# Performance work log

Hardware: AMD Instinct MI355X
Metric: run time of the kernel (lower is better)

The kernel has to match this reference:

```python
import jax, jax.numpy as jnp
import numpy as np

N = 50000      # nodes
DEG = 16       # uniform degree -> E = N*DEG edges
E = N * DEG
D_IN = 256
D_OUT = 128


def setup_inputs() -> dict:
    key = jax.random.key(0)
    k_x, k_w, k_col = jax.random.split(key, 3)
    X = jax.random.normal(k_x, (N, D_IN), dtype=jnp.float32)
    weights = jax.random.normal(k_w, (D_IN, D_OUT), dtype=jnp.float32)
    # CSR adjacency: uniform degree for simplicity; row_pointers[i] = i*DEG
    row_pointers = (jnp.arange(N + 1, dtype=jnp.int32) * DEG)
    column_index = jax.random.randint(k_col, (E,), 0, N, dtype=jnp.int32)
    # Kernel tiling metadata (unused by the math; placeholders)
    n_blk = 3125
    blockPartition = jnp.ones((n_blk,), dtype=jnp.int32)
    edgeToColumn = jnp.zeros((E,), dtype=jnp.int32)
    edgeToRow = jnp.zeros((E,), dtype=jnp.int32)
    hybrid_type = jnp.zeros((n_blk,), dtype=jnp.int32)
    row_nzr = jnp.zeros((N,), dtype=jnp.int32)
    col_nzr = jnp.zeros((E,), dtype=jnp.int32)
    return {
        "X": X,
        "weights": weights,
        "row_pointers": row_pointers,
        "column_index": column_index,
        "blockPartition": blockPartition,
        "edgeToColumn": edgeToColumn,
        "edgeToRow": edgeToRow,
        "hybrid_type": hybrid_type,
        "row_nzr": row_nzr,
        "col_nzr": col_nzr,
    }


def reference(X, weights, row_pointers, column_index, blockPartition,
              edgeToColumn, edgeToRow, hybrid_type, row_nzr, col_nzr):
    # GCNConv (fixed=0): X' = X @ W, then block-sparse SpMM A @ X' where A is the
    # unweighted CSR adjacency (sum over in-neighbors).
    Xp = jnp.matmul(X, weights)  # [N, D_OUT]
    n = X.shape[0]
    e = column_index.shape[0]
    # Recover per-edge destination row from CSR row_pointers.
    edge_dst = jnp.searchsorted(row_pointers, jnp.arange(e, dtype=row_pointers.dtype),
                                side="right").astype(jnp.int32) - 1  # [E]
    gathered = Xp[column_index]  # [E, D_OUT] irregular gather
    out = jax.ops.segment_sum(gathered, edge_dst, num_segments=n)  # [N, D_OUT]
    return out
```

## Files before the change

kernel.cpp:

```cpp
#include <hip/hip_runtime.h>
#include <hip/hip_bf16.h>


constexpr int D_IN  = 256;
constexpr int D_OUT = 128;
constexpr int BM = 128;
constexpr int BK = 32;
constexpr int LDA = BK + 8;

using short8  = __attribute__((ext_vector_type(8))) short;
using float4v = __attribute__((ext_vector_type(4))) float;

__device__ inline ushort f2bf(float f) {
    unsigned u = __float_as_uint(f);
    u = (u + 0x7FFFu + ((u >> 16) & 1u)) >> 16;
    return (ushort)u;
}

__device__ inline uint pk2bf(float lo, float hi) {
    float2 t; t.x = lo; t.y = hi;
    __hip_bfloat162 b = __float22bfloat162_rn(t);
    return *(uint*)&b;
}

__global__ __launch_bounds__(256) void prep_wt(const float* __restrict__ W,
                                               ushort* __restrict__ WT) {
    int id = blockIdx.x * 256 + threadIdx.x;
    int nn = id >> 8;
    int k  = id & 255;
    WT[nn * 256 + k] = f2bf(W[k * D_OUT + nn]);
}

__global__ __launch_bounds__(256) void gemm_xw(const float* __restrict__ X,
                                               const ushort* __restrict__ WT,
                                               ushort* __restrict__ Xp, int n) {
    __shared__ ushort Asl[BM * LDA];
    __shared__ ushort Bsl[D_OUT * LDA];
    const int tid  = threadIdx.x;
    const int wave = tid >> 6;
    const int lane = tid & 63;
    const int quad = lane >> 4;
    const int l16  = lane & 15;
    const int row0 = blockIdx.x * BM;

    float4v acc[2][8];
#pragma unroll
    for (int i = 0; i < 2; ++i)
#pragma unroll
        for (int t = 0; t < 8; ++t) acc[i][t] = (float4v){0.f, 0.f, 0.f, 0.f};

    for (int k0 = 0; k0 < D_IN; k0 += BK) {
#pragma unroll
        for (int i = 0; i < 4; ++i) {
            int idx = i * 256 + tid;
            int r = idx >> 3;
            int c4 = idx & 7;
            int row = row0 + r; if (row > n - 1) row = n - 1;
            float4 v = *(const float4*)(X + (size_t)row * D_IN + k0 + c4 * 4);
            uint2 p;
            p.x = pk2bf(v.x, v.y);
            p.y = pk2bf(v.z, v.w);
            *(uint2*)(&Asl[r * LDA + c4 * 4]) = p;
        }
#pragma unroll
        for (int i = 0; i < 2; ++i) {
            int idx = i * 256 + tid;
            int r  = idx >> 2;
            int ch = idx & 3;
            short8 v = *(const short8*)(WT + r * 256 + k0 + ch * 8);
            *(short8*)(&Bsl[r * LDA + ch * 8]) = v;
        }
        __syncthreads();

        short8 a0 = *(const short8*)(&Asl[(wave * 32 +      l16) * LDA + quad * 8]);
        short8 a1 = *(const short8*)(&Asl[(wave * 32 + 16 + l16) * LDA + quad * 8]);
#pragma unroll
        for (int t = 0; t < 8; ++t) {
            short8 b = *(const short8*)(&Bsl[(t * 16 + l16) * LDA + quad * 8]);
            acc[0][t] = __builtin_amdgcn_mfma_f32_16x16x32_bf16(a0, b, acc[0][t], 0, 0, 0);
            acc[1][t] = __builtin_amdgcn_mfma_f32_16x16x32_bf16(a1, b, acc[1][t], 0, 0, 0);
        }
        __syncthreads();
    }

#pragma unroll
    for (int rt = 0; rt < 2; ++rt) {
#pragma unroll
        for (int t = 0; t < 8; ++t) {
#pragma unroll
            for (int r = 0; r < 4; ++r) {
                int row = row0 + wave * 32 + rt * 16 + quad * 4 + r;
                if (row < n)
                    Xp[(size_t)row * D_OUT + t * 16 + l16] = f2bf(acc[rt][t][r]);
            }
        }
    }
}

__global__ __launch_bounds__(256) void spmm_agg(const ushort* __restrict__ Xp,
                                                const int* __restrict__ rowp,
                                                const int* __restrict__ colx,
                                                float* __restrict__ out, int n) {
    const int node = blockIdx.x * 4 + (threadIdx.x >> 6);
    const int lane = threadIdx.x & 63;
    if (node >= n) return;
    const int e0 = rowp[node];
    const int e1 = rowp[node + 1];
    const ushort* src = Xp + lane * 2;
    float s0 = 0.f, s1 = 0.f;
    if (e1 - e0 == 16) {
        int c[16];
#pragma unroll
        for (int i = 0; i < 16; ++i) c[i] = colx[e0 + i];
        uint v[16];
#pragma unroll
        for (int i = 0; i < 16; ++i)
            v[i] = *(const uint*)(src + (size_t)c[i] * D_OUT);
#pragma unroll
        for (int i = 0; i < 16; ++i) {
            s0 += __uint_as_float(v[i] << 16);
            s1 += __uint_as_float(v[i] & 0xFFFF0000u);
        }
    } else {
        for (int e = e0; e < e1; ++e) {
            uint v = *(const uint*)(src + (size_t)colx[e] * D_OUT);
            s0 += __uint_as_float(v << 16);
            s1 += __uint_as_float(v & 0xFFFF0000u);
        }
    }
    float2 r; r.x = s0; r.y = s1;
    *(float2*)(out + (size_t)node * D_OUT + lane * 2) = r;
}

extern "C" void kernel_launch(void* const* d_in, const int* in_sizes, int n_in,
                              void* d_out, int out_size, void* d_ws, size_t ws_size,
                              hipStream_t stream) {
    const float* X    = (const float*)d_in[0];
    const float* W    = (const float*)d_in[1];
    const int*   rowp = (const int*)d_in[2];
    const int*   colx = (const int*)d_in[3];
    float*       out  = (float*)d_out;

    ushort* WT = (ushort*)d_ws;
    ushort* Xp = (ushort*)((char*)d_ws + 65536);

    const int n = in_sizes[0] / D_IN;

    prep_wt<<<dim3(128), dim3(256), 0, stream>>>(W, WT);
    gemm_xw<<<dim3((n + BM - 1) / BM), dim3(256), 0, stream>>>(X, WT, Xp, n);
    spmm_agg<<<dim3((n + 3) / 4), dim3(256), 0, stream>>>(Xp, rowp, colx, out, n);
}
```

Baseline: 146.4 us.

## Fuse weight prep, GEMM and SpMM into one cooperative persistent kernel

Replaces three kernel launches with a single cooperative kernel that runs weight transpose, the X@W GEMM and the neighbor aggregation in sequence, separated by grid-wide syncs, using a persistent grid capped at 1024 blocks. The GEMM row tile is halved to 64 rows so each wave holds one 16-row MFMA tile, which lowers register use and allows four blocks per CU. The aim is to remove launch gaps between stages. In exchange it adds grid-sync cost, limits parallelism to the resident grid, and gives less reuse of the staged weights per tile.

```diff
diff --git a/kernel.cpp b/kernel.cpp
--- a/kernel.cpp
+++ b/kernel.cpp
@@ -1,10 +1,13 @@
 #include <hip/hip_runtime.h>
 #include <hip/hip_bf16.h>
+#include <hip/hip_cooperative_groups.h>
+
+namespace cg = cooperative_groups;
 
 
 constexpr int D_IN  = 256;
 constexpr int D_OUT = 128;
-constexpr int BM = 128;
+constexpr int BM = 64;
 constexpr int BK = 32;
 constexpr int LDA = BK + 8;
 
@@ -23,17 +26,12 @@
     return *(uint*)&b;
 }
 
-__global__ __launch_bounds__(256) void prep_wt(const float* __restrict__ W,
-                                               ushort* __restrict__ WT) {
-    int id = blockIdx.x * 256 + threadIdx.x;
-    int nn = id >> 8;
-    int k  = id & 255;
-    WT[nn * 256 + k] = f2bf(W[k * D_OUT + nn]);
-}
-
-__global__ __launch_bounds__(256) void gemm_xw(const float* __restrict__ X,
-                                               const ushort* __restrict__ WT,
-                                               ushort* __restrict__ Xp, int n) {
+__global__ __launch_bounds__(256, 4) void fused_gcn(
+    const float* __restrict__ X, const float* __restrict__ W,
+    const int* __restrict__ rowp, const int* __restrict__ colx,
+    float* __restrict__ out, ushort* __restrict__ WT,
+    ushort* __restrict__ Xp, int n)
+{
     __shared__ ushort Asl[BM * LDA];
     __shared__ ushort Bsl[D_OUT * LDA];
     const int tid  = threadIdx.x;
@@ -41,95 +39,94 @@
     const int lane = tid & 63;
     const int quad = lane >> 4;
     const int l16  = lane & 15;
-    const int row0 = blockIdx.x * BM;
+    cg::grid_group grid = cg::this_grid();
 
-    float4v acc[2][8];
+    for (int id = blockIdx.x * 256 + tid; id < D_OUT * D_IN; id += gridDim.x * 256) {
+        int nn = id >> 8;
+        int k  = id & 255;
+        WT[nn * 256 + k] = f2bf(W[k * D_OUT + nn]);
+    }
+    grid.sync();
+
+    const int ntile = (n + BM - 1) / BM;
+    for (int tile = blockIdx.x; tile < ntile; tile += gridDim.x) {
+        const int row0 = tile * BM;
+        float4v acc[8];
 #pragma unroll
-    for (int i = 0; i < 2; ++i)
+        for (int t = 0; t < 8; ++t) acc[t] = (float4v){0.f, 0.f, 0.f, 0.f};
+
+        for (int k0 = 0; k0 < D_IN; k0 += BK) {
 #pragma unroll
-        for (int t = 0; t < 8; ++t) acc[i][t] = (float4v){0.f, 0.f, 0.f, 0.f};
+            for (int i = 0; i < 2; ++i) {
+                int idx = i * 256 + tid;
+                int r   = idx >> 3;
+                int c4  = idx & 7;
+                int row = row0 + r; if (row > n - 1) row = n - 1;
+                float4 v = *(const float4*)(X + (size_t)row * D_IN + k0 + c4 * 4);
+                uint2 p;
+                p.x = pk2bf(v.x, v.y);
+                p.y = pk2bf(v.z, v.w);
+                *(uint2*)(&Asl[r * LDA + c4 * 4]) = p;
+            }
+#pragma unroll
+            for (int i = 0; i < 2; ++i) {
+                int idx = i * 256 + tid;
+                int r  = idx >> 2;
+                int ch = idx & 3;
+                short8 v = *(const short8*)(WT + r * 256 + k0 + ch * 8);
+                *(short8*)(&Bsl[r * LDA + ch * 8]) = v;
+            }
+            __syncthreads();
 
-    for (int k0 = 0; k0 < D_IN; k0 += BK) {
+            short8 a = *(const short8*)(&Asl[(wave * 16 + l16) * LDA + quad * 8]);
 #pragma unroll
-        for (int i = 0; i < 4; ++i) {
-            int idx = i * 256 + tid;
-            int r = idx >> 3;
-            int c4 = idx & 7;
-            int row = row0 + r; if (row > n - 1) row = n - 1;
-            float4 v = *(const float4*)(X + (size_t)row * D_IN + k0 + c4 * 4);
-            uint2 p;
-            p.x = pk2bf(v.x, v.y);
-            p.y = pk2bf(v.z, v.w);
-            *(uint2*)(&Asl[r * LDA + c4 * 4]) = p;
+            for (int t = 0; t < 8; ++t) {
+                short8 b = *(const short8*)(&Bsl[(t * 16 + l16) * LDA + quad * 8]);
+                acc[t] = __builtin_amdgcn_mfma_f32_16x16x32_bf16(a, b, acc[t], 0, 0, 0);
+            }
+            __syncthreads();
         }
-#pragma unroll
-        for (int i = 0; i < 2; ++i) {
-            int idx = i * 256 + tid;
-            int r  = idx >> 2;
-            int ch = idx & 3;
-            short8 v = *(const short8*)(WT + r * 256 + k0 + ch * 8);
-            *(short8*)(&Bsl[r * LDA + ch * 8]) = v;
-        }
-        __syncthreads();
 
-        short8 a0 = *(const short8*)(&Asl[(wave * 32 +      l16) * LDA + quad * 8]);
-        short8 a1 = *(const short8*)(&Asl[(wave * 32 + 16 + l16) * LDA + quad * 8]);
-#pragma unroll
-        for (int t = 0; t < 8; ++t) {
-            short8 b = *(const short8*)(&Bsl[(t * 16 + l16) * LDA + quad * 8]);
-            acc[0][t] = __builtin_amdgcn_mfma_f32_16x16x32_bf16(a0, b, acc[0][t], 0, 0, 0);
-            acc[1][t] = __builtin_amdgcn_mfma_f32_16x16x32_bf16(a1, b, acc[1][t], 0, 0, 0);
-        }
-        __syncthreads();
-    }
-
-#pragma unroll
-    for (int rt = 0; rt < 2; ++rt) {
 #pragma unroll
         for (int t = 0; t < 8; ++t) {
 #pragma unroll
             for (int r = 0; r < 4; ++r) {
-                int row = row0 + wave * 32 + rt * 16 + quad * 4 + r;
+                int row = row0 + wave * 16 + quad * 4 + r;
                 if (row < n)
-                    Xp[(size_t)row * D_OUT + t * 16 + l16] = f2bf(acc[rt][t][r]);
+                    Xp[(size_t)row * D_OUT + t * 16 + l16] = f2bf(acc[t][r]);
             }
         }
     }
-}
+    grid.sync();
 
-__global__ __launch_bounds__(256) void spmm_agg(const ushort* __restrict__ Xp,
-                                                const int* __restrict__ rowp,
-                                                const int* __restrict__ colx,
-                                                float* __restrict__ out, int n) {
-    const int node = blockIdx.x * 4 + (threadIdx.x >> 6);
-    const int lane = threadIdx.x & 63;
-    if (node >= n) return;
-    const int e0 = rowp[node];
-    const int e1 = rowp[node + 1];
     const ushort* src = Xp + lane * 2;
-    float s0 = 0.f, s1 = 0.f;
-    if (e1 - e0 == 16) {
-        int c[16];
+    for (int node = blockIdx.x * 4 + wave; node < n; node += gridDim.x * 4) {
+        const int e0 = rowp[node];
+        const int e1 = rowp[node + 1];
+        float s0 = 0.f, s1 = 0.f;
+        if (e1 - e0 == 16) {
+            int c[16];
 #pragma unroll
-        for (int i = 0; i < 16; ++i) c[i] = colx[e0 + i];
-        uint v[16];
+            for (int i = 0; i < 16; ++i) c[i] = colx[e0 + i];
+            uint v[16];
 #pragma unroll
-        for (int i = 0; i < 16; ++i)
-            v[i] = *(const uint*)(src + (size_t)c[i] * D_OUT);
+            for (int i = 0; i < 16; ++i)
+                v[i] = *(const uint*)(src + (size_t)c[i] * D_OUT);
 #pragma unroll
-        for (int i = 0; i < 16; ++i) {
-            s0 += __uint_as_float(v[i] << 16);
-            s1 += __uint_as_float(v[i] & 0xFFFF0000u);
+            for (int i = 0; i < 16; ++i) {
+                s0 += __uint_as_float(v[i] << 16);
+                s1 += __uint_as_float(v[i] & 0xFFFF0000u);
+            }
+        } else {
+            for (int e = e0; e < e1; ++e) {
+                uint v = *(const uint*)(src + (size_t)colx[e] * D_OUT);
+                s0 += __uint_as_float(v << 16);
+                s1 += __uint_as_float(v & 0xFFFF0000u);
+            }
         }
-    } else {
-        for (int e = e0; e < e1; ++e) {
-            uint v = *(const uint*)(src + (size_t)colx[e] * D_OUT);
-            s0 += __uint_as_float(v << 16);
-            s1 += __uint_as_float(v & 0xFFFF0000u);
-        }
+        float2 r2; r2.x = s0; r2.y = s1;
+        *(float2*)(out + (size_t)node * D_OUT + lane * 2) = r2;
     }
-    float2 r; r.x = s0; r.y = s1;
-    *(float2*)(out + (size_t)node * D_OUT + lane * 2) = r;
 }
 
 extern "C" void kernel_launch(void* const* d_in, const int* in_sizes, int n_in,
@@ -146,7 +143,24 @@
 
     const int n = in_sizes[0] / D_IN;
 
-    prep_wt<<<dim3(128), dim3(256), 0, stream>>>(W, WT);
-    gemm_xw<<<dim3((n + BM - 1) / BM), dim3(256), 0, stream>>>(X, WT, Xp, n);
-    spmm_agg<<<dim3((n + 3) / 4), dim3(256), 0, stream>>>(Xp, rowp, colx, out, n);
+    static int grid_blocks = 0;
+    if (grid_blocks == 0) {
+        int per_cu = 0;
+        if (hipOccupancyMaxActiveBlocksPerMultiprocessor(&per_cu, fused_gcn, 256, 0)
+                != hipSuccess || per_cu < 1)
+            per_cu = 4;
+        int num_cu = 256;
+        hipDeviceProp_t prop;
+        int dev = 0;
+        if (hipGetDevice(&dev) == hipSuccess &&
+            hipGetDeviceProperties(&prop, dev) == hipSuccess)
+            num_cu = prop.multiProcessorCount;
+        long cap = (long)per_cu * num_cu;
+        grid_blocks = (int)(cap < 1024 ? cap : 1024);
+    }
+
+    void* args[] = {(void*)&X, (void*)&W, (void*)&rowp, (void*)&colx,
+                    (void*)&out, (void*)&WT, (void*)&Xp, (void*)&n};
+    hipLaunchCooperativeKernel(fused_gcn, dim3(grid_blocks), dim3(256),
+                               args, 0, stream);
 }
```

New measurement: 323.1 us. 2.21x slower.
